# Optimization experiments

Hardware: AMD Instinct MI355X
Metric: run time of the kernel (lower is better)

## Reference

```python
import jax, jax.numpy as jnp
import numpy as np

# dims: batch, time, d_model, d_state, experts, top-k, expert hidden, regime, layers
B, T, D, S, E, K, H, R, L = 4, 512, 384, 32, 6, 2, 512, 5, 2
DI = 2 * D          # d_inner = expand * d_model
DTR = D // 16       # dt_rank = 24


def setup_inputs() -> dict:
    key = jax.random.key(0)
    ks = iter(jax.random.split(key, 48))
    def nrm(shape, s=0.02):
        return jax.random.normal(next(ks), shape, jnp.float32) * s
    inp = {}
    inp["x"] = jax.random.normal(next(ks), (B, T, D), jnp.float32)
    r = jax.random.uniform(next(ks), (B, R), jnp.float32)
    inp["regime"] = r / r.sum(-1, keepdims=True)  # regime posterior
    # FiLM conditioner
    inp["film_w1"] = nrm((R, D)); inp["film_b1"] = jnp.zeros((D,), jnp.float32)
    inp["film_w2"] = nrm((D, 2 * D)); inp["film_b2"] = jnp.zeros((2 * D,), jnp.float32)
    # SelectiveSSMBlock params, stacked over L layers
    inp["ssm_ng"] = jnp.ones((L, D), jnp.float32); inp["ssm_nb"] = jnp.zeros((L, D), jnp.float32)
    inp["in_w"] = nrm((L, D, 2 * DI))
    inp["xp_w"] = nrm((L, DI, DTR + 2 * S))
    inp["dt_w"] = nrm((L, DTR, DI)); inp["dt_b"] = jnp.zeros((L, DI), jnp.float32)
    inp["a_log_real"] = jnp.log(jnp.clip(-0.5 * jax.random.normal(next(ks), (L, DI, S), jnp.float32), 1e-4, None))
    inp["a_imag"] = 0.1 * jax.random.normal(next(ks), (L, DI, S), jnp.float32)
    inp["ssm_d"] = jnp.ones((L, DI), jnp.float32)
    inp["out_w"] = nrm((L, DI, D))
    # MoELayer params, stacked over L layers
    inp["moe_ng"] = jnp.ones((L, D), jnp.float32); inp["moe_nb"] = jnp.zeros((L, D), jnp.float32)
    inp["r_w1"] = nrm((L, D + R, D)); inp["r_b1"] = jnp.zeros((L, D), jnp.float32)
    inp["r_w2"] = nrm((L, D, E)); inp["r_b2"] = jnp.zeros((L, E), jnp.float32)
    inp["e_w1"] = nrm((L, E, D, H)); inp["e_b1"] = jnp.zeros((L, E, H), jnp.float32)
    inp["e_w2"] = nrm((L, E, H, D)); inp["e_b2"] = jnp.zeros((L, E, D), jnp.float32)
    # final norm
    inp["fin_g"] = jnp.ones((D,), jnp.float32); inp["fin_b"] = jnp.zeros((D,), jnp.float32)
    return inp


def _ln(x, g, b):
    m = x.mean(-1, keepdims=True)
    v = ((x - m) ** 2).mean(-1, keepdims=True)
    return (x - m) * jax.lax.rsqrt(v + 1e-5) * g + b


def _ssm_block(h, ng, nb, in_w, xp_w, dt_w, dt_b, alr, aim, d_vec, out_w):
    B_, T_, _ = h.shape
    xn = _ln(h, ng, nb)
    xz = xn @ in_w                        # (B,T,2*DI)
    x_ssm, z = xz[..., :DI], xz[..., DI:]
    x_dbl = x_ssm @ xp_w                  # (B,T,DTR+2S)
    dt = jax.nn.softplus(x_dbl[..., :DTR] @ dt_w + dt_b)   # (B,T,DI)
    Bp = x_dbl[..., DTR:DTR + S]          # (B,T,S)
    Cp = x_dbl[..., DTR + S:]             # (B,T,S)
    A = (-jnp.exp(alr) + 1j * aim).astype(jnp.complex64)   # (DI,S)

    def step(hc, inp):
        dt_t, bt, ct, xt = inp            # (B,DI),(B,S),(B,S),(B,DI)
        dA = jnp.exp(A[None] * dt_t[:, :, None])                       # (B,DI,S) complex
        hc = dA * hc + ((dt_t * xt)[:, :, None] * bt[:, None, :]).astype(jnp.complex64)
        # (h*C).sum(-1).real == (h.real*C).sum(-1) since C is real
        y = jnp.einsum('bds,bs->bd', hc.real, ct)
        return hc, y

    h0 = jnp.zeros((B_, DI, S), jnp.complex64)
    xsT = (jnp.moveaxis(dt, 1, 0), jnp.moveaxis(Bp, 1, 0),
           jnp.moveaxis(Cp, 1, 0), jnp.moveaxis(x_ssm, 1, 0))
    _, ysT = jax.lax.scan(step, h0, xsT)
    y = jnp.moveaxis(ysT, 0, 1) + d_vec * x_ssm   # skip term D*x
    y = y * jax.nn.silu(z)
    return h + y @ out_w                  # residual (dropout=0)


def _moe(h, regime, ng, nb, rw1, rb1, rw2, rb2, ew1, eb1, ew2, eb2):
    xn = _ln(h, ng, nb)
    B_, T_, _ = xn.shape
    reg = jnp.broadcast_to(regime[:, None, :], (B_, T_, R))
    ri = jnp.concatenate([xn, reg], -1)
    gl = jax.nn.silu(ri @ rw1 + rb1) @ rw2 + rb2    # (B,T,E)
    tv, ti = jax.lax.top_k(gl, K)
    tw = jax.nn.softmax(tv, -1)
    eo = jax.nn.silu(jnp.einsum('btd,edh->bteh', xn, ew1) + eb1)
    eo = jnp.einsum('bteh,ehd->bted', eo, ew2) + eb2   # (B,T,E,D)
    sel = jnp.take_along_axis(eo, ti[..., None], axis=2)  # (B,T,K,D)
    out = (sel * tw[..., None]).sum(2)
    gp = jax.nn.softmax(gl, -1)
    avg_p = gp.mean((0, 1))
    avg_m = jax.nn.one_hot(ti[..., 0], E, dtype=gl.dtype).mean((0, 1))
    aux = 0.01 * E * (avg_p * avg_m).sum()
    return h + out, aux


def reference(x, regime, film_w1, film_b1, film_w2, film_b2, ssm_ng, ssm_nb, in_w,
              xp_w, dt_w, dt_b, a_log_real, a_imag, ssm_d, out_w, moe_ng, moe_nb,
              r_w1, r_b1, r_w2, r_b2, e_w1, e_b1, e_w2, e_b2, fin_g, fin_b):
    # FiLM conditioning from regime posterior
    gb = jax.nn.silu(regime @ film_w1 + film_b1) @ film_w2 + film_b2
    gamma, beta = gb[:, :D], gb[:, D:]
    h = x * (gamma[:, None, :] + 1.0) + beta[:, None, :]
    aux = jnp.float32(0.0)
    for l in range(L):
        h = _ssm_block(h, ssm_ng[l], ssm_nb[l], in_w[l], xp_w[l], dt_w[l], dt_b[l],
                       a_log_real[l], a_imag[l], ssm_d[l], out_w[l])
        h, a = _moe(h, regime, moe_ng[l], moe_nb[l], r_w1[l], r_b1[l], r_w2[l], r_b2[l],
                    e_w1[l], e_b1[l], e_w2[l], e_b2[l])
        aux = aux + a
    out = _ln(h, fin_g, fin_b)
    return out, aux
```

## Files before the change

### kernel.cpp

```cpp
#include <hip/hip_runtime.h>
#include <hip/hip_bf16.h>
#include <math.h>

#define B_   4
#define T_   512
#define D_   384
#define S_   32
#define E_   6
#define H_   512
#define R_   5
#define L_   2
#define DI_  768
#define DTR_ 24
#define BT_  2048
#define XPN_ 88
#define SCH  64
#define PIT  40

typedef short s8v __attribute__((ext_vector_type(8)));
typedef float f32x4 __attribute__((ext_vector_type(4)));
typedef ushort u16x8 __attribute__((ext_vector_type(8)));

__device__ __forceinline__ float siluf(float x) { return x / (1.f + __expf(-x)); }
__device__ __forceinline__ ushort f2b(float f) {
    unsigned u = __float_as_uint(f);
    return (ushort)((u + 0x7FFFu + ((u >> 16) & 1u)) >> 16);
}
__device__ __forceinline__ float b2f(ushort h) { return __uint_as_float(((unsigned)h) << 16); }

#define CN0 1179648L
#define CN1 135168L
#define CN2 36864L
#define CN3 589824L
#define CN4 2359296L
#define CN5 2359296L
#define CN6 294912L
__global__ void conv_k(const float* __restrict__ in_w, const float* __restrict__ xp_w,
                       const float* __restrict__ dt_w, const float* __restrict__ out_w,
                       const float* __restrict__ e_w1, const float* __restrict__ e_w2,
                       const float* __restrict__ r_w1,
                       ushort* __restrict__ in_wb, ushort* __restrict__ xp_wb,
                       ushort* __restrict__ dt_wb, ushort* __restrict__ out_wb,
                       ushort* __restrict__ e1b, ushort* __restrict__ e2b,
                       ushort* __restrict__ r1h, ushort* __restrict__ r1l)
{
    const long total = CN0 + CN1 + CN2 + CN3 + CN4 + CN5 + CN6;
    long stride = (long)gridDim.x * 256;
    for (long i = (long)blockIdx.x * 256 + threadIdx.x; i < total; i += stride) {
        long j = i;
        if (j < CN0) { in_wb[j] = f2b(in_w[j]); continue; }
        j -= CN0;
        if (j < CN1) { xp_wb[j] = f2b(xp_w[j]); continue; }
        j -= CN1;
        if (j < CN2) { dt_wb[j] = f2b(dt_w[j]); continue; }
        j -= CN2;
        if (j < CN3) { out_wb[j] = f2b(out_w[j]); continue; }
        j -= CN3;
        if (j < CN4) { e1b[j] = f2b(e_w1[j]); continue; }
        j -= CN4;
        if (j < CN5) { e2b[j] = f2b(e_w2[j]); continue; }
        j -= CN5;
        {
            long l = j / 147456, rem = j - l * 147456;
            float v = r_w1[l * (long)((D_ + R_) * D_) + rem];
            ushort hv = f2b(v);
            r1h[j] = hv;
            r1l[j] = f2b(v - b2f(hv));
        }
    }
}

__global__ void film_k(const float* __restrict__ regime, const float* __restrict__ w1,
                       const float* __restrict__ b1, const float* __restrict__ w2,
                       const float* __restrict__ b2, float* __restrict__ gb,
                       float* __restrict__ stats)
{
    int b = blockIdx.x;
    int tid = threadIdx.x;
    if (b == 0 && tid < 40) stats[tid] = 0.f;
    __shared__ float t1[D_];
    if (tid < D_) {
        float a = b1[tid];
        for (int r = 0; r < R_; r++) a += regime[b * R_ + r] * w1[r * D_ + tid];
        t1[tid] = siluf(a);
    }
    __syncthreads();
    float a = b2[tid];
    for (int d = 0; d < D_; d++) a += t1[d] * w2[d * (2 * D_) + tid];
    gb[b * (2 * D_) + tid] = a;
}

__global__ void film_apply_k(const float* __restrict__ x, const float* __restrict__ gb,
                             float* __restrict__ h)
{
    int i = blockIdx.x * 256 + threadIdx.x;
    if (i >= B_ * T_ * D_) return;
    int b = i / (T_ * D_);
    int d = i % D_;
    h[i] = x[i] * (1.f + gb[b * (2 * D_) + d]) + gb[b * (2 * D_) + D_ + d];
}

template<int MODE>
__global__ __launch_bounds__(256) void ln_k(const float* __restrict__ in,
                                            const float* __restrict__ g, const float* __restrict__ b,
                                            float* __restrict__ outF,
                                            ushort* __restrict__ outH, ushort* __restrict__ outL)
{
    int row = blockIdx.x;
    int tid = threadIdx.x;
    const float* x = in + (size_t)row * D_;
    float v0 = x[tid];
    float v1 = (tid < D_ - 256) ? x[256 + tid] : 0.f;
    float s = v0 + v1, ss = v0 * v0 + v1 * v1;
#pragma unroll
    for (int o = 32; o > 0; o >>= 1) { s += __shfl_xor(s, o); ss += __shfl_xor(ss, o); }
    __shared__ float sb[8];
    int w = tid >> 6;
    if ((tid & 63) == 0) { sb[w] = s; sb[4 + w] = ss; }
    __syncthreads();
    s = sb[0] + sb[1] + sb[2] + sb[3];
    ss = sb[4] + sb[5] + sb[6] + sb[7];
    float mean = s * (1.f / D_);
    float var = ss * (1.f / D_) - mean * mean;
    float rstd = rsqrtf(var + 1e-5f);
#pragma unroll
    for (int p = 0; p < 2; p++) {
        int c = tid + p * 256;
        if (c >= D_) break;
        float v = (p ? v1 : v0);
        float o = (v - mean) * rstd * g[c] + b[c];
        size_t idx = (size_t)row * D_ + c;
        if (MODE == 0) outF[idx] = o;
        else {
            ushort hv = f2b(o);
            outH[idx] = hv;
            if (MODE == 2) outL[idx] = f2b(o - b2f(hv));
        }
    }
}

template<int OM, bool NG, bool KG, bool GATHER>
__global__ __launch_bounds__(256) void gemm_b(
    const ushort* __restrict__ A, int lda, long aOff,
    const ushort* __restrict__ W, int ldw, long wOff,
    float* __restrict__ C, int ldc, long cOff,
    ushort* __restrict__ Cb, int ldcb, long cbOff, int nb16,
    const float* __restrict__ bias, long bOff,
    const int* __restrict__ glist, const int* __restrict__ gcnt,
    int N, int K, int act, int acc)
{
    __shared__ __align__(16) ushort As[2][64 * PIT];
    __shared__ __align__(16) ushort Bs[2][64 * PIT];
    const int z = blockIdx.z;
    const int bm = blockIdx.y * 64, bn = blockIdx.x * 64;
    int cnt = 0;
    if (gcnt) { cnt = gcnt[z]; if (bm >= cnt) return; }
    const int tid = threadIdx.x, w = tid >> 6, lane = tid & 63;
    const int wm = (w >> 1) * 32, wn = (w & 1) * 32;
    const int l16 = lane & 15, lk = lane >> 4;
    const int r0 = tid >> 2, c0 = (tid & 3) * 8;
    const ushort* Ab;
    if (GATHER) {
        int gr = bm + r0;
        int t_idx = (gr < cnt) ? glist[(size_t)z * BT_ + gr] : 0;
        Ab = A + (size_t)t_idx * lda;
    } else {
        Ab = A + (size_t)z * aOff + (size_t)(bm + r0) * lda;
    }
    const ushort* Wb = W + (size_t)z * wOff;

    f32x4 accv[2][2];
#pragma unroll
    for (int i = 0; i < 2; i++)
#pragma unroll
        for (int j = 0; j < 2; j++) accv[i][j] = (f32x4)0.f;

    u16x8 arg;
    ushort wrg[8];
    auto LOADA = [&](int k0) {
        arg = *reinterpret_cast<const u16x8*>(Ab + k0 + c0);
    };
    auto LOADW = [&](int k0) {
#pragma unroll
        for (int i = 0; i < 8; i++) {
            int kk = k0 + w * 8 + i;
            bool ok = (!KG || kk < K) && (!NG || (bn + lane) < N);
            wrg[i] = ok ? Wb[(size_t)kk * ldw + bn + lane] : (ushort)0;
        }
    };
    auto STORE = [&](int buf) {
        *reinterpret_cast<u16x8*>(&As[buf][r0 * PIT + c0]) = arg;
        *reinterpret_cast<ushort4*>(&Bs[buf][lane * PIT + w * 8]) =
            make_ushort4(wrg[0], wrg[1], wrg[2], wrg[3]);
        *reinterpret_cast<ushort4*>(&Bs[buf][lane * PIT + w * 8 + 4]) =
            make_ushort4(wrg[4], wrg[5], wrg[6], wrg[7]);
    };

    LOADA(0); LOADW(0); STORE(0);
    __syncthreads();
    const int NIT = (K + 31) / 32;
    for (int it = 0; it < NIT; it++) {
        int cur = it & 1;
        bool more = (it + 1 < NIT);
        if (more) { LOADA((it + 1) * 32); LOADW((it + 1) * 32); }
        s8v af[2], bfr[2];
#pragma unroll
        for (int mf = 0; mf < 2; mf++)
            af[mf] = *reinterpret_cast<const s8v*>(&As[cur][(wm + mf * 16 + l16) * PIT + lk * 8]);
#pragma unroll
        for (int nf = 0; nf < 2; nf++)
            bfr[nf] = *reinterpret_cast<const s8v*>(&Bs[cur][(wn + nf * 16 + l16) * PIT + lk * 8]);
#pragma unroll
        for (int mf = 0; mf < 2; mf++)
#pragma unroll
            for (int nf = 0; nf < 2; nf++)
                accv[mf][nf] = __builtin_amdgcn_mfma_f32_16x16x32_bf16(af[mf], bfr[nf], accv[mf][nf], 0, 0, 0);
        if (more) { STORE(cur ^ 1); __syncthreads(); }
    }

    const float* biasb = bias ? bias + (size_t)z * bOff : nullptr;
#pragma unroll
    for (int mf = 0; mf < 2; mf++) {
#pragma unroll
        for (int nf = 0; nf < 2; nf++) {
            int col = bn + wn + nf * 16 + l16;
            if (NG && col >= N) continue;
#pragma unroll
            for (int r = 0; r < 4; r++) {
                int rr = bm + wm + mf * 16 + lk * 4 + r;
                if (gcnt && rr >= cnt) continue;
                float v = accv[mf][nf][r];
                if (biasb) v += biasb[col];
                if (act == 1) v = siluf(v);
                else if (act == 2) v = (v > 0.f) ? v + log1pf(__expf(-v)) : log1pf(__expf(v));
                if (OM == 0 || OM == 2) {
                    float* Cz = C + (size_t)z * cOff;
                    size_t ci = (size_t)rr * ldc + col;
                    Cz[ci] = acc ? (Cz[ci] + v) : v;
                }
                if (OM >= 1) {
                    if (col < nb16)
                        (Cb + (size_t)z * cbOff)[(size_t)rr * ldcb + col] = f2b(v);
                }
            }
        }
    }
}

__global__ __launch_bounds__(256) void gemm3_k(
    const ushort* __restrict__ Ah, const ushort* __restrict__ Al, int lda,
    const ushort* __restrict__ Wh, const ushort* __restrict__ Wl, int ldw,
    float* __restrict__ C,
    const float* __restrict__ bias, const float* __restrict__ rowbias,
    int N, int K)
{
    __shared__ __align__(16) ushort sAh[64 * PIT], sAl[64 * PIT];
    __shared__ __align__(16) ushort sWh[128 * PIT], sWl[128 * PIT];
    const int bm = blockIdx.y * 64, bn = blockIdx.x * 128;
    const int tid = threadIdx.x, w = tid >> 6, lane = tid & 63;
    const int wm = (w >> 1) * 32, wn = (w & 1) * 64;
    const int l16 = lane & 15, lk = lane >> 4;
    const int r0 = tid >> 2, c0 = (tid & 3) * 8;
    f32x4 accv[2][4];
#pragma unroll
    for (int i = 0; i < 2; i++)
#pragma unroll
        for (int j = 0; j < 4; j++) accv[i][j] = (f32x4)0.f;

    for (int k0 = 0; k0 < K; k0 += 32) {
        *reinterpret_cast<u16x8*>(&sAh[r0 * PIT + c0]) =
            *reinterpret_cast<const u16x8*>(Ah + (size_t)(bm + r0) * lda + k0 + c0);
        *reinterpret_cast<u16x8*>(&sAl[r0 * PIT + c0]) =
            *reinterpret_cast<const u16x8*>(Al + (size_t)(bm + r0) * lda + k0 + c0);
#pragma unroll
        for (int hh = 0; hh < 2; hh++) {
            int n = hh * 64 + lane;
            ushort th[8], tl[8];
#pragma unroll
            for (int i = 0; i < 8; i++) {
                int kk = k0 + w * 8 + i;
                th[i] = Wh[(size_t)kk * ldw + bn + n];
                tl[i] = Wl[(size_t)kk * ldw + bn + n];
            }
            *reinterpret_cast<ushort4*>(&sWh[n * PIT + w * 8])     = make_ushort4(th[0], th[1], th[2], th[3]);
            *reinterpret_cast<ushort4*>(&sWh[n * PIT + w * 8 + 4]) = make_ushort4(th[4], th[5], th[6], th[7]);
            *reinterpret_cast<ushort4*>(&sWl[n * PIT + w * 8])     = make_ushort4(tl[0], tl[1], tl[2], tl[3]);
            *reinterpret_cast<ushort4*>(&sWl[n * PIT + w * 8 + 4]) = make_ushort4(tl[4], tl[5], tl[6], tl[7]);
        }
        __syncthreads();
        s8v ah[2], al[2], bh[4], bl[4];
#pragma unroll
        for (int mf = 0; mf < 2; mf++) {
            ah[mf] = *reinterpret_cast<const s8v*>(&sAh[(wm + mf * 16 + l16) * PIT + lk * 8]);
            al[mf] = *reinterpret_cast<const s8v*>(&sAl[(wm + mf * 16 + l16) * PIT + lk * 8]);
        }
#pragma unroll
        for (int nf = 0; nf < 4; nf++) {
            bh[nf] = *reinterpret_cast<const s8v*>(&sWh[(wn + nf * 16 + l16) * PIT + lk * 8]);
            bl[nf] = *reinterpret_cast<const s8v*>(&sWl[(wn + nf * 16 + l16) * PIT + lk * 8]);
        }
#pragma unroll
        for (int mf = 0; mf < 2; mf++)
#pragma unroll
            for (int nf = 0; nf < 4; nf++) {
                accv[mf][nf] = __builtin_amdgcn_mfma_f32_16x16x32_bf16(ah[mf], bh[nf], accv[mf][nf], 0, 0, 0);
                accv[mf][nf] = __builtin_amdgcn_mfma_f32_16x16x32_bf16(ah[mf], bl[nf], accv[mf][nf], 0, 0, 0);
                accv[mf][nf] = __builtin_amdgcn_mfma_f32_16x16x32_bf16(al[mf], bh[nf], accv[mf][nf], 0, 0, 0);
            }
        __syncthreads();
    }
#pragma unroll
    for (int mf = 0; mf < 2; mf++)
#pragma unroll
        for (int nf = 0; nf < 4; nf++) {
            int col = bn + wn + nf * 16 + l16;
#pragma unroll
            for (int r = 0; r < 4; r++) {
                int rr = bm + wm + mf * 16 + lk * 4 + r;
                float v = accv[mf][nf][r] + bias[col] + rowbias[(rr / T_) * N + col];
                C[(size_t)rr * N + col] = siluf(v);
            }
        }
}

__global__ __launch_bounds__(128) void scan_k(
    const float* __restrict__ dtb, const float* __restrict__ xz, const float* __restrict__ xdbl,
    const float* __restrict__ alr, const float* __restrict__ aim, const float* __restrict__ dvecp,
    ushort* __restrict__ ygb)
{
    int p = blockIdx.x;
    int blk = (p & 7) * 96 + (p >> 3);
    int b = blk / 192;
    int dbase = (blk % 192) * 4;
    int tid = threadIdx.x;
    int ch = tid >> 5;
    int s = tid & 31;
    int d = dbase + ch;
    __shared__ __align__(16) float sBC[SCH][64];
    __shared__ __align__(16) float sdt[SCH][4], sx[SCH][4], sz[SCH][4];
    __shared__ float sacc[SCH * 4][33];
    float negA = -__expf(alr[d * S_ + s]);
    float aimv = aim[d * S_ + s];
    float4 dv4 = *reinterpret_cast<const float4*>(dvecp + dbase);
    float dvc[4] = {dv4.x, dv4.y, dv4.z, dv4.w};
    float hre = 0.f, him = 0.f;
    const float* dtp = dtb + (size_t)b * T_ * DI_;
    const float* xzp = xz + (size_t)b * T_ * (2 * DI_);
    const float* xdp = xdbl + (size_t)b * T_ * XPN_;
    ushort* ygp = ygb + (size_t)b * T_ * DI_;

    for (int c = 0; c < T_ / SCH; c++) {
        int tc = c * SCH;
        __syncthreads();
#pragma unroll
        for (int i = 0; i < 8; i++) {
            int idx = tid + i * 128;
            int tt = idx >> 4, jj = (idx & 15) * 4;
            *reinterpret_cast<float4*>(&sBC[tt][jj]) =
                *reinterpret_cast<const float4*>(xdp + (size_t)(tc + tt) * XPN_ + DTR_ + jj);
        }
        if (tid < 64) {
            *reinterpret_cast<float4*>(&sdt[tid][0]) =
                *reinterpret_cast<const float4*>(dtp + (size_t)(tc + tid) * DI_ + dbase);
            *reinterpret_cast<float4*>(&sz[tid][0]) =
                *reinterpret_cast<const float4*>(xzp + (size_t)(tc + tid) * (2 * DI_) + DI_ + dbase);
        } else {
            int tt = tid - 64;
            *reinterpret_cast<float4*>(&sx[tt][0]) =
                *reinterpret_cast<const float4*>(xzp + (size_t)(tc + tt) * (2 * DI_) + dbase);
        }
        __syncthreads();

        float dt0 = sdt[0][ch], x0 = sx[0][ch], B0 = sBC[0][s], C0 = sBC[0][32 + s];
        float dt1 = sdt[1][ch], x1 = sx[1][ch], B1 = sBC[1][s], C1 = sBC[1][32 + s];
#pragma unroll 4
        for (int t = 0; t < SCH; t++) {
            float dt2 = 0.f, x2 = 0.f, B2 = 0.f, C2 = 0.f;
            if (t + 2 < SCH) {
                dt2 = sdt[t + 2][ch]; x2 = sx[t + 2][ch];
                B2 = sBC[t + 2][s];  C2 = sBC[t + 2][32 + s];
            }
            float e = __expf(negA * dt0);
            float sn, cs;
            __sincosf(aimv * dt0, &sn, &cs);
            float dre = e * cs, dim = e * sn;
            float u = dt0 * x0 * B0;
            float nre = fmaf(dre, hre, fmaf(-dim, him, u));
            him = fmaf(dre, him, dim * hre);
            hre = nre;
            sacc[t * 4 + ch][s] = hre * C0;
            dt0 = dt1; x0 = x1; B0 = B1; C0 = C1;
            dt1 = dt2; x1 = x2; B1 = B2; C1 = C2;
        }
        __syncthreads();

#pragma unroll
        for (int p2 = 0; p2 < 2; p2++) {
            int r = tid + p2 * 128;
            float acc = 0.f;
#pragma unroll
            for (int s2 = 0; s2 < 32; s2++) acc += sacc[r][s2];
            int t = r >> 2, cch = r & 3;
            float xv = sx[t][cch], zv = sz[t][cch];
            float y = (acc + dvc[cch] * xv) * siluf(zv);
            ygp[(size_t)(tc + t) * DI_ + dbase + cch] = f2b(y);
        }
    }
}

__global__ void regc_k(const float* __restrict__ regime, const float* __restrict__ rw1l,
                       float* __restrict__ regc)
{
    int i = blockIdx.x * 256 + threadIdx.x;
    if (i >= B_ * D_) return;
    int b = i / D_, d = i % D_;
    float a = 0.f;
    for (int r = 0; r < R_; r++) a += regime[b * R_ + r] * rw1l[(D_ + r) * D_ + d];
    regc[i] = a;
}

__global__ __launch_bounds__(256) void gl_k(const float* __restrict__ hmid,
                                            const float* __restrict__ rw2l,
                                            const float* __restrict__ rb2l, float* __restrict__ gl)
{
    int pid = blockIdx.x * 16 + (threadIdx.x >> 4);
    int li = threadIdx.x & 15;
    int t = pid / E_, e = pid - t * E_;
    const float* hp = hmid + (size_t)t * D_;
    float a = 0.f;
#pragma unroll 4
    for (int j = 0; j < D_ / 16; j++) {
        int k = li + j * 16;
        a += hp[k] * rw2l[k * E_ + e];
    }
#pragma unroll
    for (int o = 8; o > 0; o >>= 1) a += __shfl_xor(a, o, 16);
    if (li == 0) gl[t * E_ + e] = a + rb2l[e];
}

__global__ __launch_bounds__(256) void router_k(const float* __restrict__ gl,
                                                float* __restrict__ tw, int* __restrict__ ti,
                                                float* __restrict__ statL)
{
    __shared__ float s_p[E_];
    __shared__ float s_c[E_];
    int tid = threadIdx.x;
    if (tid < E_) { s_p[tid] = 0.f; s_c[tid] = 0.f; }
    __syncthreads();
    int t = blockIdx.x * 256 + tid;
    if (t < BT_) {
        float g[E_];
        for (int e = 0; e < E_; e++) g[e] = gl[t * E_ + e];
        int i0 = 0; float v0 = g[0];
        for (int e = 1; e < E_; e++) if (g[e] > v0) { v0 = g[e]; i0 = e; }
        int i1 = -1; float v1 = -1e30f;
        for (int e = 0; e < E_; e++) if (e != i0 && g[e] > v1) { v1 = g[e]; i1 = e; }
        float e1 = __expf(v1 - v0);
        float inv = 1.f / (1.f + e1);
        tw[t * 2] = inv; tw[t * 2 + 1] = e1 * inv;
        ti[t * 2] = i0;  ti[t * 2 + 1] = i1;
        float p[E_], se = 0.f;
        for (int e = 0; e < E_; e++) { p[e] = __expf(g[e] - v0); se += p[e]; }
        float rse = 1.f / se;
        for (int e = 0; e < E_; e++) atomicAdd(&s_p[e], p[e] * rse);
        atomicAdd(&s_c[i0], 1.f);
    }
    __syncthreads();
    if (tid < E_) { atomicAdd(&statL[tid], s_p[tid]); atomicAdd(&statL[8 + tid], s_c[tid]); }
}

__global__ __launch_bounds__(1024) void moe_assign_k(const int* __restrict__ ti,
                                                     int* __restrict__ glist,
                                                     int* __restrict__ tpos,
                                                     int* __restrict__ cnt)
{
    __shared__ int scnt[E_];
    int tid = threadIdx.x;
    if (tid < E_) scnt[tid] = 0;
    __syncthreads();
    for (int t = tid; t < BT_; t += 1024) {
#pragma unroll
        for (int kk = 0; kk < 2; kk++) {
            int e = ti[2 * t + kk];
            int pos = atomicAdd(&scnt[e], 1);
            glist[e * BT_ + pos] = t;
            tpos[2 * t + kk] = e * BT_ + pos;
        }
    }
    __syncthreads();
    if (tid < E_) cnt[tid] = scnt[tid];
}

__global__ void sel_k(const ushort* __restrict__ eodb, const float* __restrict__ tw,
                      const int* __restrict__ tpos, float* __restrict__ h)
{
    int i = blockIdx.x * 256 + threadIdx.x;
    if (i >= BT_ * D_) return;
    int t = i / D_, d = i % D_;
    int p0 = tpos[t * 2], p1 = tpos[t * 2 + 1];
    h[i] += tw[t * 2]     * b2f(eodb[(size_t)p0 * D_ + d])
          + tw[t * 2 + 1] * b2f(eodb[(size_t)p1 * D_ + d]);
}

__global__ void write_aux_k(const float* __restrict__ stats, float* __restrict__ out)
{
    if (threadIdx.x == 0 && blockIdx.x == 0) {
        float aux = 0.f;
        for (int l = 0; l < L_; l++) {
            float s = 0.f;
            for (int e = 0; e < E_; e++) s += stats[l * 16 + e] * stats[l * 16 + 8 + e];
            aux += 0.01f * (float)E_ * s / ((float)BT_ * (float)BT_);
        }
        out[BT_ * D_] = aux;
    }
}

extern "C" void kernel_launch(void* const* d_in, const int* in_sizes, int n_in,
                              void* d_out, int out_size, void* d_ws, size_t ws_size,
                              hipStream_t stream)
{
    const float* x       = (const float*)d_in[0];
    const float* regime  = (const float*)d_in[1];
    const float* film_w1 = (const float*)d_in[2];
    const float* film_b1 = (const float*)d_in[3];
    const float* film_w2 = (const float*)d_in[4];
    const float* film_b2 = (const float*)d_in[5];
    const float* ssm_ng  = (const float*)d_in[6];
    const float* ssm_nb  = (const float*)d_in[7];
    const float* in_w    = (const float*)d_in[8];
    const float* xp_w    = (const float*)d_in[9];
    const float* dt_w    = (const float*)d_in[10];
    const float* dt_b    = (const float*)d_in[11];
    const float* alr     = (const float*)d_in[12];
    const float* aimp    = (const float*)d_in[13];
    const float* ssm_d   = (const float*)d_in[14];
    const float* out_w   = (const float*)d_in[15];
    const float* moe_ng  = (const float*)d_in[16];
    const float* moe_nb  = (const float*)d_in[17];
    const float* r_w1    = (const float*)d_in[18];
    const float* r_b1    = (const float*)d_in[19];
    const float* r_w2    = (const float*)d_in[20];
    const float* r_b2    = (const float*)d_in[21];
    const float* e_w1    = (const float*)d_in[22];
    const float* e_b1    = (const float*)d_in[23];
    const float* e_w2    = (const float*)d_in[24];
    const float* e_b2    = (const float*)d_in[25];
    const float* fin_g   = (const float*)d_in[26];
    const float* fin_b   = (const float*)d_in[27];

    float* ws = (float*)d_ws;
    size_t o = 0;
    float*  h      = ws + o; o += 786432;
    float*  stats  = ws + o; o += 64;
    ushort* xnH    = (ushort*)(ws + o); o += 393216;
    ushort* xnL    = (ushort*)(ws + o); o += 393216;
    float*  regc   = ws + o; o += 1536;
    float*  gl     = ws + o; o += 12288;
    float*  tw     = ws + o; o += 4096;
    int*    ti     = (int*)(ws + o); o += 4096;
    int*    glist  = (int*)(ws + o); o += 12288;
    int*    tpos   = (int*)(ws + o); o += 4096;
    int*    cnt    = (int*)(ws + o); o += 16;
    ushort* in_wb  = (ushort*)(ws + o); o += 589824;
    ushort* xp_wb  = (ushort*)(ws + o); o += 67584;
    ushort* dt_wb  = (ushort*)(ws + o); o += 18432;
    ushort* out_wb = (ushort*)(ws + o); o += 294912;
    ushort* e1b    = (ushort*)(ws + o); o += 1179648;
    ushort* e2b    = (ushort*)(ws + o); o += 1179648;
    ushort* r1h    = (ushort*)(ws + o); o += 147456;
    ushort* r1l    = (ushort*)(ws + o); o += 147456;
    float*  xz    = ws + o;
    ushort* xzb   = (ushort*)(ws + o + 3145728);
    float*  xdbl  = ws + o + 3932160;
    ushort* xdblb = (ushort*)(ws + o + 4112384);
    float*  dtb   = ws + o + 4145152;
    ushort* ygb   = (ushort*)(ws + o + 5718016);
    float*  hmid  = ws + o;
    ushort* eohb  = (ushort*)(ws + o + 786432);
    ushort* eodb  = (ushort*)(ws + o + 3932160);
    float*  gb    = ws + o;

    conv_k<<<2048, 256, 0, stream>>>(in_w, xp_w, dt_w, out_w, e_w1, e_w2, r_w1,
                                     in_wb, xp_wb, dt_wb, out_wb, e1b, e2b, r1h, r1l);
    film_k<<<B_, 2 * D_, 0, stream>>>(regime, film_w1, film_b1, film_w2, film_b2, gb, stats);
    film_apply_k<<<(B_ * T_ * D_ + 255) / 256, 256, 0, stream>>>(x, gb, h);

    for (int l = 0; l < L_; l++) {
        ln_k<1><<<BT_, 256, 0, stream>>>(h, ssm_ng + l * D_, ssm_nb + l * D_, nullptr, xnH, nullptr);
        gemm_b<2, false, false, false><<<dim3(24, 32), 256, 0, stream>>>(
            xnH, D_, 0, in_wb + (size_t)l * 589824, 2 * DI_, 0,
            xz, 2 * DI_, 0, xzb, DI_, 0, DI_,
            nullptr, 0, nullptr, nullptr, 2 * DI_, D_, 0, 0);
        gemm_b<2, true, false, false><<<dim3(2, 32), 256, 0, stream>>>(
            xzb, DI_, 0, xp_wb + (size_t)l * 67584, XPN_, 0,
            xdbl, XPN_, 0, xdblb, 32, 0, 32,
            nullptr, 0, nullptr, nullptr, XPN_, DI_, 0, 0);
        gemm_b<0, false, true, false><<<dim3(12, 32), 256, 0, stream>>>(
            xdblb, 32, 0, dt_wb + (size_t)l * 18432, DI_, 0,
            dtb, DI_, 0, nullptr, 0, 0, 0,
            dt_b + l * DI_, 0, nullptr, nullptr, DI_, DTR_, 2, 0);
        scan_k<<<B_ * 192, 128, 0, stream>>>(
            dtb, xz, xdbl, alr + (size_t)l * DI_ * S_, aimp + (size_t)l * DI_ * S_,
            ssm_d + l * DI_, ygb);
        gemm_b<0, false, false, false><<<dim3(6, 32), 256, 0, stream>>>(
            ygb, DI_, 0, out_wb + (size_t)l * 294912, D_, 0,
            h, D_, 0, nullptr, 0, 0, 0,
            nullptr, 0, nullptr, nullptr, D_, DI_, 0, 1);

        ln_k<2><<<BT_, 256, 0, stream>>>(h, moe_ng + l * D_, moe_nb + l * D_, nullptr, xnH, xnL);
        regc_k<<<(B_ * D_ + 255) / 256, 256, 0, stream>>>(regime, r_w1 + (size_t)l * (D_ + R_) * D_, regc);
        gemm3_k<<<dim3(3, 32), 256, 0, stream>>>(
            xnH, xnL, D_, r1h + (size_t)l * 147456, r1l + (size_t)l * 147456, D_,
            hmid, r_b1 + l * D_, regc, D_, D_);
        gl_k<<<BT_ * E_ / 16, 256, 0, stream>>>(hmid, r_w2 + (size_t)l * D_ * E_, r_b2 + l * E_, gl);
        router_k<<<BT_ / 256, 256, 0, stream>>>(gl, tw, ti, stats + l * 16);
        moe_assign_k<<<1, 1024, 0, stream>>>(ti, glist, tpos, cnt);
        gemm_b<1, false, false, true><<<dim3(8, 32, 6), 256, 0, stream>>>(
            xnH, D_, 0, e1b + (size_t)l * 1179648, H_, (long)D_ * H_,
            nullptr, 0, 0, eohb, H_, (long)BT_ * H_, H_,
            e_b1 + (size_t)l * E_ * H_, H_, glist, cnt, H_, D_, 1, 0);
        gemm_b<1, false, false, false><<<dim3(6, 32, 6), 256, 0, stream>>>(
            eohb, H_, (long)BT_ * H_, e2b + (size_t)l * 1179648, D_, (long)H_ * D_,
            nullptr, 0, 0, eodb, D_, (long)BT_ * D_, D_,
            e_b2 + (size_t)l * E_ * D_, D_, nullptr, cnt, D_, H_, 0, 0);
        sel_k<<<(BT_ * D_ + 255) / 256, 256, 0, stream>>>(eodb, tw, tpos, h);
    }

    ln_k<0><<<BT_, 256, 0, stream>>>(h, fin_g, fin_b, (float*)d_out, nullptr, nullptr);
    write_aux_k<<<1, 64, 0, stream>>>(stats, (float*)d_out);
}
```

Before: 588.8 us.

## Fuse MoE combine with next LayerNorm, merge router kernels, interleave scan inputs

```diff
diff --git a/kernel.cpp b/kernel.cpp
--- a/kernel.cpp
+++ b/kernel.cpp
@@ -16,6 +16,8 @@
 #define XPN_ 88
 #define SCH  64
 #define PIT  40
+#define SPD  10
+#define SPB  66
 
 typedef short s8v __attribute__((ext_vector_type(8)));
 typedef float f32x4 __attribute__((ext_vector_type(4)));
@@ -139,6 +141,55 @@
     }
 }
 
+template<int MODE>
+__global__ __launch_bounds__(256) void selln_k(float* __restrict__ h,
+                                               const ushort* __restrict__ eodb,
+                                               const float* __restrict__ tw,
+                                               const int* __restrict__ tpos,
+                                               const float* __restrict__ g, const float* __restrict__ b,
+                                               float* __restrict__ outF,
+                                               ushort* __restrict__ outH, ushort* __restrict__ outL)
+{
+    int row = blockIdx.x;
+    int tid = threadIdx.x;
+    float* hp = h + (size_t)row * D_;
+    int p0 = tpos[row * 2], p1 = tpos[row * 2 + 1];
+    float w0 = tw[row * 2], w1 = tw[row * 2 + 1];
+    const ushort* e0 = eodb + (size_t)p0 * D_;
+    const ushort* e1 = eodb + (size_t)p1 * D_;
+    float v0 = hp[tid] + w0 * b2f(e0[tid]) + w1 * b2f(e1[tid]);
+    float v1 = 0.f;
+    if (tid < D_ - 256) v1 = hp[256 + tid] + w0 * b2f(e0[256 + tid]) + w1 * b2f(e1[256 + tid]);
+    hp[tid] = v0;
+    if (tid < D_ - 256) hp[256 + tid] = v1;
+    float s = v0 + v1, ss = v0 * v0 + v1 * v1;
+#pragma unroll
+    for (int o = 32; o > 0; o >>= 1) { s += __shfl_xor(s, o); ss += __shfl_xor(ss, o); }
+    __shared__ float sb[8];
+    int w = tid >> 6;
+    if ((tid & 63) == 0) { sb[w] = s; sb[4 + w] = ss; }
+    __syncthreads();
+    s = sb[0] + sb[1] + sb[2] + sb[3];
+    ss = sb[4] + sb[5] + sb[6] + sb[7];
+    float mean = s * (1.f / D_);
+    float var = ss * (1.f / D_) - mean * mean;
+    float rstd = rsqrtf(var + 1e-5f);
+#pragma unroll
+    for (int p = 0; p < 2; p++) {
+        int c = tid + p * 256;
+        if (c >= D_) break;
+        float v = (p ? v1 : v0);
+        float o = (v - mean) * rstd * g[c] + b[c];
+        size_t idx = (size_t)row * D_ + c;
+        if (MODE == 0) outF[idx] = o;
+        else {
+            ushort hv = f2b(o);
+            outH[idx] = hv;
+            if (MODE == 2) outL[idx] = f2b(o - b2f(hv));
+        }
+    }
+}
+
 template<int OM, bool NG, bool KG, bool GATHER>
 __global__ __launch_bounds__(256) void gemm_b(
     const ushort* __restrict__ A, int lda, long aOff,
@@ -238,9 +289,17 @@
                     size_t ci = (size_t)rr * ldc + col;
                     Cz[ci] = acc ? (Cz[ci] + v) : v;
                 }
-                if (OM >= 1) {
+                if (OM == 1 || OM == 2) {
                     if (col < nb16)
                         (Cb + (size_t)z * cbOff)[(size_t)rr * ldcb + col] = f2b(v);
+                }
+                if (OM == 3) {
+                    if (col < nb16)
+                        Cb[(size_t)rr * ldcb + col] = f2b(v);
+                    if (col >= 24) {
+                        int q = col - 24;
+                        C[(size_t)rr * 64 + ((q < 32) ? (2 * q) : (2 * (q - 32) + 1))] = v;
+                    }
                 }
             }
         }
@@ -251,7 +310,8 @@
     const ushort* __restrict__ Ah, const ushort* __restrict__ Al, int lda,
     const ushort* __restrict__ Wh, const ushort* __restrict__ Wl, int ldw,
     float* __restrict__ C,
-    const float* __restrict__ bias, const float* __restrict__ rowbias,
+    const float* __restrict__ bias,
+    const float* __restrict__ regime, const float* __restrict__ rw1t,
     int N, int K)
 {
     __shared__ __align__(16) ushort sAh[64 * PIT], sAl[64 * PIT];
@@ -309,22 +369,26 @@
             }
         __syncthreads();
     }
+    const float* rg = regime + (bm / T_) * R_;
 #pragma unroll
     for (int mf = 0; mf < 2; mf++)
 #pragma unroll
         for (int nf = 0; nf < 4; nf++) {
             int col = bn + wn + nf * 16 + l16;
+            float rb = 0.f;
+#pragma unroll
+            for (int r = 0; r < R_; r++) rb += rg[r] * rw1t[r * D_ + col];
 #pragma unroll
             for (int r = 0; r < 4; r++) {
                 int rr = bm + wm + mf * 16 + lk * 4 + r;
-                float v = accv[mf][nf][r] + bias[col] + rowbias[(rr / T_) * N + col];
+                float v = accv[mf][nf][r] + bias[col] + rb;
                 C[(size_t)rr * N + col] = siluf(v);
             }
         }
 }
 
 __global__ __launch_bounds__(128) void scan_k(
-    const float* __restrict__ dtb, const float* __restrict__ xz, const float* __restrict__ xdbl,
+    const float* __restrict__ dtb, const float* __restrict__ xz, const float* __restrict__ bcint,
     const float* __restrict__ alr, const float* __restrict__ aim, const float* __restrict__ dvecp,
     ushort* __restrict__ ygb)
 {
@@ -336,8 +400,8 @@
     int ch = tid >> 5;
     int s = tid & 31;
     int d = dbase + ch;
-    __shared__ __align__(16) float sBC[SCH][64];
-    __shared__ __align__(16) float sdt[SCH][4], sx[SCH][4], sz[SCH][4];
+    __shared__ __align__(16) float sdx[64 * SPD];
+    __shared__ __align__(16) float sbc[64 * SPB];
     __shared__ float sacc[SCH * 4][33];
     float negA = -__expf(alr[d * S_ + s]);
     float aimv = aim[d * S_ + s];
@@ -346,77 +410,70 @@
     float hre = 0.f, him = 0.f;
     const float* dtp = dtb + (size_t)b * T_ * DI_;
     const float* xzp = xz + (size_t)b * T_ * (2 * DI_);
-    const float* xdp = xdbl + (size_t)b * T_ * XPN_;
+    const float* bcp = bcint + (size_t)b * T_ * 64;
     ushort* ygp = ygb + (size_t)b * T_ * DI_;
 
     for (int c = 0; c < T_ / SCH; c++) {
         int tc = c * SCH;
         __syncthreads();
+        if (tid < 64) {
+            int t = tid;
+            float4 d4 = *reinterpret_cast<const float4*>(dtp + (size_t)(tc + t) * DI_ + dbase);
+            float4 x4 = *reinterpret_cast<const float4*>(xzp + (size_t)(tc + t) * (2 * DI_) + dbase);
+            float dd[4] = {d4.x, d4.y, d4.z, d4.w};
+            float xx[4] = {x4.x, x4.y, x4.z, x4.w};
+#pragma unroll
+            for (int k = 0; k < 4; k++)
+                *reinterpret_cast<float2*>(&sdx[t * SPD + 2 * k]) = make_float2(dd[k], xx[k]);
+        }
 #pragma unroll
         for (int i = 0; i < 8; i++) {
             int idx = tid + i * 128;
-            int tt = idx >> 4, jj = (idx & 15) * 4;
-            *reinterpret_cast<float4*>(&sBC[tt][jj]) =
-                *reinterpret_cast<const float4*>(xdp + (size_t)(tc + tt) * XPN_ + DTR_ + jj);
-        }
-        if (tid < 64) {
-            *reinterpret_cast<float4*>(&sdt[tid][0]) =
-                *reinterpret_cast<const float4*>(dtp + (size_t)(tc + tid) * DI_ + dbase);
-            *reinterpret_cast<float4*>(&sz[tid][0]) =
-                *reinterpret_cast<const float4*>(xzp + (size_t)(tc + tid) * (2 * DI_) + DI_ + dbase);
-        } else {
-            int tt = tid - 64;
-            *reinterpret_cast<float4*>(&sx[tt][0]) =
-                *reinterpret_cast<const float4*>(xzp + (size_t)(tc + tt) * (2 * DI_) + dbase);
+            int tt = idx >> 4, q = idx & 15;
+            *reinterpret_cast<float4*>(&sbc[tt * SPB + 4 * q]) =
+                *reinterpret_cast<const float4*>(bcp + (size_t)(tc + tt) * 64 + 4 * q);
         }
         __syncthreads();
 
-        float dt0 = sdt[0][ch], x0 = sx[0][ch], B0 = sBC[0][s], C0 = sBC[0][32 + s];
-        float dt1 = sdt[1][ch], x1 = sx[1][ch], B1 = sBC[1][s], C1 = sBC[1][32 + s];
+        const float* dxr = &sdx[2 * ch];
+        const float* bcr = &sbc[2 * s];
+        float2 dx0 = *reinterpret_cast<const float2*>(dxr);
+        float2 bc0 = *reinterpret_cast<const float2*>(bcr);
+        float2 dx1 = *reinterpret_cast<const float2*>(dxr + SPD);
+        float2 bc1 = *reinterpret_cast<const float2*>(bcr + SPB);
 #pragma unroll 4
         for (int t = 0; t < SCH; t++) {
-            float dt2 = 0.f, x2 = 0.f, B2 = 0.f, C2 = 0.f;
+            float2 dx2 = make_float2(0.f, 0.f), bc2 = dx2;
             if (t + 2 < SCH) {
-                dt2 = sdt[t + 2][ch]; x2 = sx[t + 2][ch];
-                B2 = sBC[t + 2][s];  C2 = sBC[t + 2][32 + s];
+                dx2 = *reinterpret_cast<const float2*>(dxr + (t + 2) * SPD);
+                bc2 = *reinterpret_cast<const float2*>(bcr + (t + 2) * SPB);
             }
-            float e = __expf(negA * dt0);
+            float e = __expf(negA * dx0.x);
             float sn, cs;
-            __sincosf(aimv * dt0, &sn, &cs);
+            __sincosf(aimv * dx0.x, &sn, &cs);
             float dre = e * cs, dim = e * sn;
-            float u = dt0 * x0 * B0;
+            float u = dx0.x * dx0.y * bc0.x;
             float nre = fmaf(dre, hre, fmaf(-dim, him, u));
             him = fmaf(dre, him, dim * hre);
             hre = nre;
-            sacc[t * 4 + ch][s] = hre * C0;
-            dt0 = dt1; x0 = x1; B0 = B1; C0 = C1;
-            dt1 = dt2; x1 = x2; B1 = B2; C1 = C2;
+            sacc[t * 4 + ch][s] = hre * bc0.y;
+            dx0 = dx1; bc0 = bc1; dx1 = dx2; bc1 = bc2;
         }
         __syncthreads();
 
 #pragma unroll
         for (int p2 = 0; p2 < 2; p2++) {
             int r = tid + p2 * 128;
+            int t = r >> 2, cch = r & 3;
             float acc = 0.f;
 #pragma unroll
             for (int s2 = 0; s2 < 32; s2++) acc += sacc[r][s2];
-            int t = r >> 2, cch = r & 3;
-            float xv = sx[t][cch], zv = sz[t][cch];
+            float xv = sdx[t * SPD + 2 * cch + 1];
+            float zv = xzp[(size_t)(tc + t) * (2 * DI_) + DI_ + dbase + cch];
             float y = (acc + dvc[cch] * xv) * siluf(zv);
             ygp[(size_t)(tc + t) * DI_ + dbase + cch] = f2b(y);
         }
     }
-}
-
-__global__ void regc_k(const float* __restrict__ regime, const float* __restrict__ rw1l,
-                       float* __restrict__ regc)
-{
-    int i = blockIdx.x * 256 + threadIdx.x;
-    if (i >= B_ * D_) return;
-    int b = i / D_, d = i % D_;
-    float a = 0.f;
-    for (int r = 0; r < R_; r++) a += regime[b * R_ + r] * rw1l[(D_ + r) * D_ + d];
-    regc[i] = a;
 }
 
 __global__ __launch_bounds__(256) void gl_k(const float* __restrict__ hmid,
@@ -438,17 +495,19 @@
     if (li == 0) gl[t * E_ + e] = a + rb2l[e];
 }
 
-__global__ __launch_bounds__(256) void router_k(const float* __restrict__ gl,
-                                                float* __restrict__ tw, int* __restrict__ ti,
-                                                float* __restrict__ statL)
-{
-    __shared__ float s_p[E_];
-    __shared__ float s_c[E_];
+__global__ __launch_bounds__(1024) void router_assign_k(const float* __restrict__ gl,
+                                                        float* __restrict__ tw,
+                                                        int* __restrict__ glist,
+                                                        int* __restrict__ tpos,
+                                                        int* __restrict__ cnt,
+                                                        float* __restrict__ statL)
+{
+    __shared__ float s_p[E_], s_c[E_];
+    __shared__ int scnt[E_];
     int tid = threadIdx.x;
-    if (tid < E_) { s_p[tid] = 0.f; s_c[tid] = 0.f; }
+    if (tid < E_) { s_p[tid] = 0.f; s_c[tid] = 0.f; scnt[tid] = 0; }
     __syncthreads();
-    int t = blockIdx.x * 256 + tid;
-    if (t < BT_) {
+    for (int t = tid; t < BT_; t += 1024) {
         float g[E_];
         for (int e = 0; e < E_; e++) g[e] = gl[t * E_ + e];
         int i0 = 0; float v0 = g[0];
@@ -458,48 +517,24 @@
         float e1 = __expf(v1 - v0);
         float inv = 1.f / (1.f + e1);
         tw[t * 2] = inv; tw[t * 2 + 1] = e1 * inv;
-        ti[t * 2] = i0;  ti[t * 2 + 1] = i1;
-        float p[E_], se = 0.f;
-        for (int e = 0; e < E_; e++) { p[e] = __expf(g[e] - v0); se += p[e]; }
+        int pos0 = atomicAdd(&scnt[i0], 1);
+        glist[i0 * BT_ + pos0] = t;
+        tpos[2 * t] = i0 * BT_ + pos0;
+        int pos1 = atomicAdd(&scnt[i1], 1);
+        glist[i1 * BT_ + pos1] = t;
+        tpos[2 * t + 1] = i1 * BT_ + pos1;
+        float pb[E_], se = 0.f;
+        for (int e = 0; e < E_; e++) { pb[e] = __expf(g[e] - v0); se += pb[e]; }
         float rse = 1.f / se;
-        for (int e = 0; e < E_; e++) atomicAdd(&s_p[e], p[e] * rse);
+        for (int e = 0; e < E_; e++) atomicAdd(&s_p[e], pb[e] * rse);
         atomicAdd(&s_c[i0], 1.f);
     }
     __syncthreads();
-    if (tid < E_) { atomicAdd(&statL[tid], s_p[tid]); atomicAdd(&statL[8 + tid], s_c[tid]); }
-}
-
-__global__ __launch_bounds__(1024) void moe_assign_k(const int* __restrict__ ti,
-                                                     int* __restrict__ glist,
-                                                     int* __restrict__ tpos,
-                                                     int* __restrict__ cnt)
-{
-    __shared__ int scnt[E_];
-    int tid = threadIdx.x;
-    if (tid < E_) scnt[tid] = 0;
-    __syncthreads();
-    for (int t = tid; t < BT_; t += 1024) {
-#pragma unroll
-        for (int kk = 0; kk < 2; kk++) {
-            int e = ti[2 * t + kk];
-            int pos = atomicAdd(&scnt[e], 1);
-            glist[e * BT_ + pos] = t;
-            tpos[2 * t + kk] = e * BT_ + pos;
-        }
-    }
-    __syncthreads();
-    if (tid < E_) cnt[tid] = scnt[tid];
-}
-
-__global__ void sel_k(const ushort* __restrict__ eodb, const float* __restrict__ tw,
-                      const int* __restrict__ tpos, float* __restrict__ h)
-{
-    int i = blockIdx.x * 256 + threadIdx.x;
-    if (i >= BT_ * D_) return;
-    int t = i / D_, d = i % D_;
-    int p0 = tpos[t * 2], p1 = tpos[t * 2 + 1];
-    h[i] += tw[t * 2]     * b2f(eodb[(size_t)p0 * D_ + d])
-          + tw[t * 2 + 1] * b2f(eodb[(size_t)p1 * D_ + d]);
+    if (tid < E_) {
+        cnt[tid] = scnt[tid];
+        statL[tid] = s_p[tid];
+        statL[8 + tid] = s_c[tid];
+    }
 }
 
 __global__ void write_aux_k(const float* __restrict__ stats, float* __restrict__ out)
@@ -554,10 +589,8 @@
     float*  stats  = ws + o; o += 64;
     ushort* xnH    = (ushort*)(ws + o); o += 393216;
     ushort* xnL    = (ushort*)(ws + o); o += 393216;
-    float*  regc   = ws + o; o += 1536;
     float*  gl     = ws + o; o += 12288;
     float*  tw     = ws + o; o += 4096;
-    int*    ti     = (int*)(ws + o); o += 4096;
     int*    glist  = (int*)(ws + o); o += 12288;
     int*    tpos   = (int*)(ws + o); o += 4096;
     int*    cnt    = (int*)(ws + o); o += 16;
@@ -571,10 +604,10 @@
     ushort* r1l    = (ushort*)(ws + o); o += 147456;
     float*  xz    = ws + o;
     ushort* xzb   = (ushort*)(ws + o + 3145728);
-    float*  xdbl  = ws + o + 3932160;
-    ushort* xdblb = (ushort*)(ws + o + 4112384);
-    float*  dtb   = ws + o + 4145152;
-    ushort* ygb   = (ushort*)(ws + o + 5718016);
+    float*  bcint = ws + o + 3932160;
+    ushort* xdblb = (ushort*)(ws + o + 4063232);
+    float*  dtb   = ws + o + 4096000;
+    ushort* ygb   = (ushort*)(ws + o + 5668864);
     float*  hmid  = ws + o;
     ushort* eohb  = (ushort*)(ws + o + 786432);
     ushort* eodb  = (ushort*)(ws + o + 3932160);
@@ -586,21 +619,22 @@
     film_apply_k<<<(B_ * T_ * D_ + 255) / 256, 256, 0, stream>>>(x, gb, h);
 
     for (int l = 0; l < L_; l++) {
-        ln_k<1><<<BT_, 256, 0, stream>>>(h, ssm_ng + l * D_, ssm_nb + l * D_, nullptr, xnH, nullptr);
+        if (l == 0)
+            ln_k<1><<<BT_, 256, 0, stream>>>(h, ssm_ng, ssm_nb, nullptr, xnH, nullptr);
         gemm_b<2, false, false, false><<<dim3(24, 32), 256, 0, stream>>>(
             xnH, D_, 0, in_wb + (size_t)l * 589824, 2 * DI_, 0,
             xz, 2 * DI_, 0, xzb, DI_, 0, DI_,
             nullptr, 0, nullptr, nullptr, 2 * DI_, D_, 0, 0);
-        gemm_b<2, true, false, false><<<dim3(2, 32), 256, 0, stream>>>(
+        gemm_b<3, true, false, false><<<dim3(2, 32), 256, 0, stream>>>(
             xzb, DI_, 0, xp_wb + (size_t)l * 67584, XPN_, 0,
-            xdbl, XPN_, 0, xdblb, 32, 0, 32,
+            bcint, 64, 0, xdblb, 32, 0, 32,
             nullptr, 0, nullptr, nullptr, XPN_, DI_, 0, 0);
         gemm_b<0, false, true, false><<<dim3(12, 32), 256, 0, stream>>>(
             xdblb, 32, 0, dt_wb + (size_t)l * 18432, DI_, 0,
             dtb, DI_, 0, nullptr, 0, 0, 0,
             dt_b + l * DI_, 0, nullptr, nullptr, DI_, DTR_, 2, 0);
         scan_k<<<B_ * 192, 128, 0, stream>>>(
-            dtb, xz, xdbl, alr + (size_t)l * DI_ * S_, aimp + (size_t)l * DI_ * S_,
+            dtb, xz, bcint, alr + (size_t)l * DI_ * S_, aimp + (size_t)l * DI_ * S_,
             ssm_d + l * DI_, ygb);
         gemm_b<0, false, false, false><<<dim3(6, 32), 256, 0, stream>>>(
             ygb, DI_, 0, out_wb + (size_t)l * 294912, D_, 0,
@@ -608,13 +642,13 @@
             nullptr, 0, nullptr, nullptr, D_, DI_, 0, 1);
 
         ln_k<2><<<BT_, 256, 0, stream>>>(h, moe_ng + l * D_, moe_nb + l * D_, nullptr, xnH, xnL);
-        regc_k<<<(B_ * D_ + 255) / 256, 256, 0, stream>>>(regime, r_w1 + (size_t)l * (D_ + R_) * D_, regc);
         gemm3_k<<<dim3(3, 32), 256, 0, stream>>>(
             xnH, xnL, D_, r1h + (size_t)l * 147456, r1l + (size_t)l * 147456, D_,
-            hmid, r_b1 + l * D_, regc, D_, D_);
+            hmid, r_b1 + l * D_,
+            regime, r_w1 + (size_t)l * ((D_ + R_) * D_) + (size_t)D_ * D_,
+            D_, D_);
         gl_k<<<BT_ * E_ / 16, 256, 0, stream>>>(hmid, r_w2 + (size_t)l * D_ * E_, r_b2 + l * E_, gl);
-        router_k<<<BT_ / 256, 256, 0, stream>>>(gl, tw, ti, stats + l * 16);
-        moe_assign_k<<<1, 1024, 0, stream>>>(ti, glist, tpos, cnt);
+        router_assign_k<<<1, 1024, 0, stream>>>(gl, tw, glist, tpos, cnt, stats + l * 16);
         gemm_b<1, false, false, true><<<dim3(8, 32, 6), 256, 0, stream>>>(
             xnH, D_, 0, e1b + (size_t)l * 1179648, H_, (long)D_ * H_,
             nullptr, 0, 0, eohb, H_, (long)BT_ * H_, H_,
@@ -623,9 +657,13 @@
             eohb, H_, (long)BT_ * H_, e2b + (size_t)l * 1179648, D_, (long)H_ * D_,
             nullptr, 0, 0, eodb, D_, (long)BT_ * D_, D_,
             e_b2 + (size_t)l * E_ * D_, D_, nullptr, cnt, D_, H_, 0, 0);
-        sel_k<<<(BT_ * D_ + 255) / 256, 256, 0, stream>>>(eodb, tw, tpos, h);
-    }
-
-    ln_k<0><<<BT_, 256, 0, stream>>>(h, fin_g, fin_b, (float*)d_out, nullptr, nullptr);
+        if (l < L_ - 1)
+            selln_k<1><<<BT_, 256, 0, stream>>>(h, eodb, tw, tpos,
+                ssm_ng + (l + 1) * D_, ssm_nb + (l + 1) * D_, nullptr, xnH, nullptr);
+        else
+            selln_k<0><<<BT_, 256, 0, stream>>>(h, eodb, tw, tpos,
+                fin_g, fin_b, (float*)d_out, nullptr, nullptr);
+    }
+
     write_aux_k<<<1, 64, 0, stream>>>(stats, (float*)d_out);
 }
```

Result: slower. 612.6 us (+4.0%).
